# Optimization experiments

Measured on AMD Instinct MI355X. Metric: run time of the kernel, lower is better.

## Reference

```python
import jax, jax.numpy as jnp
import numpy as np

C = 256
HEADS = 8
HD = C // HEADS
SCALE = HD ** -0.5


def conv1x1(x, W, b):
    # x: [B,C_in,H,W], W: [C_out,C_in], b: [C_out]
    return jnp.einsum('oc,bchw->bohw', W, x) + b[None, :, None, None]


def setup_inputs() -> dict:
    key = jax.random.key(0)
    ks = jax.random.split(key, 12)
    B, H, Wd = 2, 48, 48
    s = C ** -0.5
    return {
        'x': jax.random.normal(ks[0], (B, C, H, Wd), jnp.float32),
        'uncertainty': jax.random.uniform(ks[1], (B, 1, H, Wd), jnp.float32),
        'Wq': jax.random.normal(ks[2], (C, C), jnp.float32) * s,
        'bq': jnp.zeros((C,), jnp.float32),
        'Wk': jax.random.normal(ks[3], (C, C), jnp.float32) * s,
        'bk': jnp.zeros((C,), jnp.float32),
        'Wv': jax.random.normal(ks[4], (C, C), jnp.float32) * s,
        'bv': jnp.zeros((C,), jnp.float32),
        'Wg': jax.random.normal(ks[5], (C, 1), jnp.float32),
        'bg': jnp.zeros((C,), jnp.float32),
        'Wo': jax.random.normal(ks[6], (C, C), jnp.float32) * s,
        'bo': jnp.zeros((C,), jnp.float32),
    }


def reference(x, uncertainty, Wq, bq, Wk, bk, Wv, bv, Wg, bg, Wo, bo):
    B, _, H, Wd = x.shape
    N = H * Wd
    # uncertainty gate (1x1 conv from 1 channel to C channels)
    uw = conv1x1(uncertainty, Wg, bg)            # [B,C,H,W]
    gated_x = x * (1.0 - uw)
    q = conv1x1(gated_x, Wq, bq).reshape(B, HEADS, HD, N)
    k = conv1x1(gated_x, Wk, bk).reshape(B, HEADS, HD, N)
    v = conv1x1(x, Wv, bv).reshape(B, HEADS, HD, N)
    # scores: [B,h,N,N] (query tokens n, key tokens m)
    scores = jnp.einsum('bhdn,bhdm->bhnm', q, k) * SCALE
    u_flat = uncertainty.reshape(B, 1, 1, N)      # mask over key axis
    scores = scores * (1.0 - u_flat)
    attn = jax.nn.softmax(scores, axis=-1)
    out = jnp.einsum('bhnm,bhdm->bhdn', attn, v)  # [B,h,hd,N]
    out = out.reshape(B, C, H, Wd)
    out = conv1x1(out, Wo, bo)
    return out + x
```

## Files before the change

### kernel.cpp

```cpp
#include <hip/hip_runtime.h>
#include <hip/hip_bf16.h>

typedef float f32x4 __attribute__((ext_vector_type(4)));
typedef __bf16 bf16x8 __attribute__((ext_vector_type(8)));
typedef __bf16 bf16x4 __attribute__((ext_vector_type(4)));
typedef short s16x4 __attribute__((ext_vector_type(4)));

constexpr int C = 256;
constexpr int N = 2304;
constexpr int T = 2 * N;

#if __has_builtin(__builtin_amdgcn_exp2f)
#define EXP2F(x) __builtin_amdgcn_exp2f(x)
#else
#define EXP2F(x) exp2f(x)
#endif

__device__ __forceinline__ bf16x8 load_bf8(const __bf16* p) {
    return *reinterpret_cast<const bf16x8*>(p);
}

__device__ __forceinline__ f32x4 mfma32(bf16x8 a, bf16x8 b, f32x4 c) {
    return __builtin_amdgcn_mfma_f32_16x16x32_bf16(a, b, c, 0, 0, 0);
}

#if __has_builtin(__builtin_amdgcn_mfma_f32_16x16x16bf16_1k)
__device__ __forceinline__ f32x4 mfma16(bf16x4 a, bf16x4 b, f32x4 c) {
    return __builtin_amdgcn_mfma_f32_16x16x16bf16_1k(
        __builtin_bit_cast(s16x4, a), __builtin_bit_cast(s16x4, b), c, 0, 0, 0);
}
#else
__device__ __forceinline__ f32x4 mfma16(bf16x4 a, bf16x4 b, f32x4 c) {
    f32x4 d;
    asm volatile("v_mfma_f32_16x16x16_bf16 %0, %1, %2, %3"
                 : "=v"(d) : "v"(a), "v"(b), "v"(c));
    return d;
}
#endif

__device__ __forceinline__ void gload_lds16(const __bf16* g, __bf16* l) {
    __builtin_amdgcn_global_load_lds(
        (const __attribute__((address_space(1))) void*)g,
        (__attribute__((address_space(3))) void*)l, 16, 0, 0);
}

#define VMCNT4() asm volatile("s_waitcnt vmcnt(4)" ::: "memory")
#define VMCNT0() asm volatile("s_waitcnt vmcnt(0)" ::: "memory")
#define LGKM0()  asm volatile("s_waitcnt lgkmcnt(0)" ::: "memory")

__global__ void wconv_kernel(const float* __restrict__ Wq, const float* __restrict__ Wk,
                             const float* __restrict__ Wv, const float* __restrict__ Wo,
                             __bf16* __restrict__ Wb) {
    const float* srcs[4] = {Wq, Wk, Wv, Wo};
    int m = blockIdx.x >> 6;
    int idx = (blockIdx.x & 63) * 256 + threadIdx.x;
    float4 v = reinterpret_cast<const float4*>(srcs[m])[idx];
    bf16x4 o = { (__bf16)v.x, (__bf16)v.y, (__bf16)v.z, (__bf16)v.w };
    reinterpret_cast<bf16x4*>(Wb + m * 65536)[idx] = o;
}

__global__ void prep_kernel(const float* __restrict__ x, const float* __restrict__ u,
                            const float* __restrict__ Wg, const float* __restrict__ bg,
                            __bf16* __restrict__ xT, __bf16* __restrict__ gxT) {
    __shared__ float tile[64][65];
    int b = blockIdx.z, c0 = blockIdx.y * 64, n0 = blockIdx.x * 64;
    int t = threadIdx.x;
    const float* xp = x + (b * C + c0) * N + n0;
    #pragma unroll
    for (int r = 0; r < 16; ++r) {
        int cl = r * 4 + (t >> 6);
        int nl = t & 63;
        tile[cl][nl] = xp[cl * N + nl];
    }
    __syncthreads();
    int cq = (t & 15) * 4;
    #pragma unroll
    for (int it = 0; it < 4; ++it) {
        int nl = it * 16 + (t >> 4);
        float uv = u[b * N + n0 + nl];
        bf16x4 xo, go;
        #pragma unroll
        for (int j = 0; j < 4; ++j) {
            int c = c0 + cq + j;
            float xv = tile[cq + j][nl];
            float gate = 1.0f - (Wg[c] * uv + bg[c]);
            xo[j] = (__bf16)xv;
            go[j] = (__bf16)(xv * gate);
        }
        int tok = b * N + n0 + nl;
        *reinterpret_cast<bf16x4*>(xT + (long)tok * C + c0 + cq) = xo;
        *reinterpret_cast<bf16x4*>(gxT + (long)tok * C + c0 + cq) = go;
    }
}

__global__ __launch_bounds__(256) void qkv_kernel(const __bf16* __restrict__ Wb,
    const __bf16* __restrict__ xT, const __bf16* __restrict__ gxT,
    const float* __restrict__ bq, const float* __restrict__ bk, const float* __restrict__ bv,
    const float* __restrict__ u,
    __bf16* __restrict__ Q, __bf16* __restrict__ K, __bf16* __restrict__ V) {
    int proj = blockIdx.z;
    int o0 = blockIdx.y * 64;
    int t0 = blockIdx.x * 32;
    int wave = threadIdx.x >> 6, lane = threadIdx.x & 63;
    int g = lane >> 4, r = lane & 15;
    int ow = o0 + wave * 16;
    const __bf16* W = Wb + proj * 65536;
    const __bf16* inp = (proj == 2) ? xT : gxT;
    f32x4 acc[2] = {};
    for (int k = 0; k < 8; ++k) {
        bf16x8 a = load_bf8(W + (ow + r) * C + k * 32 + g * 8);
        #pragma unroll
        for (int tb = 0; tb < 2; ++tb) {
            bf16x8 bfr = load_bf8(inp + (long)(t0 + tb * 16 + r) * C + k * 32 + g * 8);
            acc[tb] = mfma32(a, bfr, acc[tb]);
        }
    }
    const float* bias = (proj == 0) ? bq : (proj == 1) ? bk : bv;
    float bvw[4];
    #pragma unroll
    for (int i = 0; i < 4; ++i) bvw[i] = bias[ow + g * 4 + i];
    int h = ow >> 5, d0 = (ow & 31) + g * 4;
    const float SC = 0.17677669529663687f * 1.4426950408889634f;
    #pragma unroll
    for (int tb = 0; tb < 2; ++tb) {
        int t = t0 + tb * 16 + r;
        int b = t / N, n = t % N;
        if (proj == 2) {
            #pragma unroll
            for (int i = 0; i < 4; ++i)
                V[((long)(b * 8 + h) * 32 + d0 + i) * N + n] = (__bf16)(acc[tb][i] + bvw[i]);
        } else {
            bf16x4 outv;
            if (proj == 1) {
                float scale = SC * (1.0f - u[t]);
                #pragma unroll
                for (int i = 0; i < 4; ++i) outv[i] = (__bf16)((acc[tb][i] + bvw[i]) * scale);
            } else {
                #pragma unroll
                for (int i = 0; i < 4; ++i) outv[i] = (__bf16)(acc[tb][i] + bvw[i]);
            }
            __bf16* dst = (proj == 0) ? Q : K;
            *reinterpret_cast<bf16x4*>(dst + ((long)(b * 8 + h) * N + n) * 32 + d0) = outv;
        }
    }
}

__global__ __launch_bounds__(128) void attn_kernel(const __bf16* __restrict__ Q,
    const __bf16* __restrict__ K, const __bf16* __restrict__ V,
    __bf16* __restrict__ aoT) {
    __shared__ __bf16 sK[3][2048];
    __shared__ __bf16 sV[3][2048];
    int id = blockIdx.x;
    int xcd = id & 7, j = id >> 3;
    int bh = xcd + 8 * (j / 72);
    int qblk = j % 72;
    int tid = threadIdx.x;
    int wave = tid >> 6, lane = tid & 63;
    int g = lane >> 4, r = lane & 15;
    int q0w = qblk * 32 + wave * 16;
    const __bf16* Qg = Q + (long)bh * N * 32;
    const __bf16* Kg = K + (long)bh * N * 32;
    const __bf16* Vg = V + (long)bh * 32 * N;
    bf16x8 qf = load_bf8(Qg + (q0w + r) * 32 + g * 8);
    long ka = (long)tid * 8;
    int rrA = tid >> 3;
    int clA = (tid & 7) ^ ((tid >> 4) & 7);
    long va = (long)rrA * N + clA * 8;
    int so = wave * 512;
    auto STAGE = [&](long m0, __bf16* kd, __bf16* vd) {
        gload_lds16(Kg + m0 * 32 + ka,          kd + so);
        gload_lds16(Kg + m0 * 32 + 1024 + ka,   kd + 1024 + so);
        gload_lds16(Vg + va + m0,               vd + so);
        gload_lds16(Vg + va + 16 * N + m0,      vd + 1024 + so);
    };
    __bf16 *kA = &sK[0][0], *kB = &sK[1][0], *kC = &sK[2][0];
    __bf16 *vA = &sV[0][0], *vB = &sV[1][0], *vC = &sV[2][0];
    bf16x4 onesv;
    #pragma unroll
    for (int i = 0; i < 4; ++i) onesv[i] = (__bf16)1.0f;
    f32x4 oa0 = {}, oa1 = {}, oal = {};
    STAGE(0, kA, vA);
    STAGE(64, kB, vB);
    int k2r = (r >> 1) & 7;
    for (int t = 0; t < 36; ++t) {
        LGKM0();
        if (t < 34) { VMCNT4(); } else { VMCNT0(); }
        __builtin_amdgcn_s_barrier();
        if (t < 34) STAGE((long)(t + 2) * 64, kC, vC);
        bf16x8 kc0 = load_bf8(kA + (0 * 16 + r) * 32 + g * 8);
        bf16x8 kc1 = load_bf8(kA + (1 * 16 + r) * 32 + g * 8);
        bf16x8 kc2 = load_bf8(kA + (2 * 16 + r) * 32 + g * 8);
        bf16x8 kc3 = load_bf8(kA + (3 * 16 + r) * 32 + g * 8);
        bf16x4 vf[4][2];
        #pragma unroll
        for (int tt = 0; tt < 4; ++tt) {
            int pg = (((tt * 2 + (g >> 1)) ^ k2r) << 1) | (g & 1);
            #pragma unroll
            for (int dt = 0; dt < 2; ++dt)
                vf[tt][dt] = *reinterpret_cast<const bf16x4*>(
                    vA + (dt * 16 + r) * 64 + pg * 4);
        }
        f32x4 z = {};
        __builtin_amdgcn_s_setprio(1);
        f32x4 s0 = mfma32(kc0, qf, z);
        f32x4 s1 = mfma32(kc1, qf, z);
        f32x4 s2 = mfma32(kc2, qf, z);
        f32x4 s3 = mfma32(kc3, qf, z);
        __builtin_amdgcn_s_setprio(0);
        bf16x4 pa0, pa1, pa2, pa3;
        #pragma unroll
        for (int i = 0; i < 4; ++i) pa0[i] = (__bf16)EXP2F(s0[i]);
        #pragma unroll
        for (int i = 0; i < 4; ++i) pa1[i] = (__bf16)EXP2F(s1[i]);
        #pragma unroll
        for (int i = 0; i < 4; ++i) pa2[i] = (__bf16)EXP2F(s2[i]);
        #pragma unroll
        for (int i = 0; i < 4; ++i) pa3[i] = (__bf16)EXP2F(s3[i]);
        __builtin_amdgcn_s_setprio(1);
        oa0 = mfma16(vf[0][0], pa0, oa0);
        oa1 = mfma16(vf[0][1], pa0, oa1);
        oal = mfma16(onesv,    pa0, oal);
        oa0 = mfma16(vf[1][0], pa1, oa0);
        oa1 = mfma16(vf[1][1], pa1, oa1);
        oal = mfma16(onesv,    pa1, oal);
        oa0 = mfma16(vf[2][0], pa2, oa0);
        oa1 = mfma16(vf[2][1], pa2, oa1);
        oal = mfma16(onesv,    pa2, oal);
        oa0 = mfma16(vf[3][0], pa3, oa0);
        oa1 = mfma16(vf[3][1], pa3, oa1);
        oal = mfma16(onesv,    pa3, oal);
        __builtin_amdgcn_s_setprio(0);
        __bf16* tk = kA; kA = kB; kB = kC; kC = tk;
        __bf16* tv = vA; vA = vB; vB = vC; vC = tv;
    }
    float inv = 1.0f / oal[0];
    int b = bh >> 3, h = bh & 7;
    long tok = (long)b * N + q0w + r;
    bf16x4 ov0, ov1;
    #pragma unroll
    for (int i = 0; i < 4; ++i) ov0[i] = (__bf16)(oa0[i] * inv);
    #pragma unroll
    for (int i = 0; i < 4; ++i) ov1[i] = (__bf16)(oa1[i] * inv);
    *reinterpret_cast<bf16x4*>(aoT + tok * C + h * 32 + g * 4) = ov0;
    *reinterpret_cast<bf16x4*>(aoT + tok * C + h * 32 + 16 + g * 4) = ov1;
}

__global__ __launch_bounds__(256) void outp_kernel(const __bf16* __restrict__ Wb,
    const __bf16* __restrict__ aoT, const float* __restrict__ bo,
    const float* __restrict__ x, float* __restrict__ out) {
    int o0 = blockIdx.y * 64;
    int t0 = blockIdx.x * 32;
    int wave = threadIdx.x >> 6, lane = threadIdx.x & 63;
    int g = lane >> 4, r = lane & 15;
    int ow = o0 + wave * 16;
    const __bf16* W = Wb + 3 * 65536;
    f32x4 acc[2] = {};
    for (int k = 0; k < 8; ++k) {
        bf16x8 a = load_bf8(W + (ow + r) * C + k * 32 + g * 8);
        #pragma unroll
        for (int tb = 0; tb < 2; ++tb) {
            bf16x8 bfr = load_bf8(aoT + (long)(t0 + tb * 16 + r) * C + k * 32 + g * 8);
            acc[tb] = mfma32(a, bfr, acc[tb]);
        }
    }
    float bvw[4];
    #pragma unroll
    for (int i = 0; i < 4; ++i) bvw[i] = bo[ow + g * 4 + i];
    #pragma unroll
    for (int tb = 0; tb < 2; ++tb) {
        int t = t0 + tb * 16 + r;
        int b = t / N, n = t % N;
        #pragma unroll
        for (int i = 0; i < 4; ++i) {
            long idx = ((long)b * C + ow + g * 4 + i) * N + n;
            out[idx] = acc[tb][i] + bvw[i] + x[idx];
        }
    }
}

extern "C" void kernel_launch(void* const* d_in, const int* in_sizes, int n_in,
                              void* d_out, int out_size, void* d_ws, size_t ws_size,
                              hipStream_t stream) {
    const float* x  = (const float*)d_in[0];
    const float* u  = (const float*)d_in[1];
    const float* Wq = (const float*)d_in[2];
    const float* bq = (const float*)d_in[3];
    const float* Wk = (const float*)d_in[4];
    const float* bk = (const float*)d_in[5];
    const float* Wv = (const float*)d_in[6];
    const float* bv = (const float*)d_in[7];
    const float* Wg = (const float*)d_in[8];
    const float* bg = (const float*)d_in[9];
    const float* Wo = (const float*)d_in[10];
    const float* bo = (const float*)d_in[11];
    float* out = (float*)d_out;

    char* ws = (char*)d_ws;
    size_t off = 0;
    auto alloc = [&](size_t bytes) {
        char* p = ws + off;
        off += (bytes + 255) & ~(size_t)255;
        return p;
    };
    __bf16* Wb  = (__bf16*)alloc((size_t)4 * 65536 * 2);
    __bf16* xT  = (__bf16*)alloc((size_t)T * C * 2);
    __bf16* gxT = (__bf16*)alloc((size_t)T * C * 2);
    __bf16* Qb  = (__bf16*)alloc((size_t)16 * N * 32 * 2);
    __bf16* Kb  = (__bf16*)alloc((size_t)16 * N * 32 * 2);
    __bf16* Vb  = (__bf16*)alloc((size_t)16 * N * 32 * 2);
    __bf16* aoT = (__bf16*)alloc((size_t)T * C * 2);

    wconv_kernel<<<256, 256, 0, stream>>>(Wq, Wk, Wv, Wo, Wb);
    prep_kernel<<<dim3(36, 4, 2), 256, 0, stream>>>(x, u, Wg, bg, xT, gxT);
    qkv_kernel<<<dim3(144, 4, 3), 256, 0, stream>>>(Wb, xT, gxT, bq, bk, bv, u, Qb, Kb, Vb);
    attn_kernel<<<1152, 128, 0, stream>>>(Qb, Kb, Vb, aoT);
    outp_kernel<<<dim3(144, 4), 256, 0, stream>>>(Wb, aoT, bo, x, out);
}
```

Measured before the change: 78.97 us.

## Split attention key range across wave pairs and shrink prep/outp tiles

The attention kernel now runs 256 threads per block. Two wave pairs each process half of the key sequence with their own double-buffered LDS stages, and their partial outputs and row sums are combined through LDS at the end. This gives each block more parallelism and shortens the serial loop, at the cost of an extra reduction, a full vmcnt(0) wait each iteration instead of a three-stage pipeline, and larger LDS use. The prep and output projection kernels are also retiled to smaller per-block work so more blocks launch.

```diff
diff --git a/kernel.cpp b/kernel.cpp
--- a/kernel.cpp
+++ b/kernel.cpp
@@ -44,7 +44,6 @@
         (__attribute__((address_space(3))) void*)l, 16, 0, 0);
 }
 
-#define VMCNT4() asm volatile("s_waitcnt vmcnt(4)" ::: "memory")
 #define VMCNT0() asm volatile("s_waitcnt vmcnt(0)" ::: "memory")
 #define LGKM0()  asm volatile("s_waitcnt lgkmcnt(0)" ::: "memory")
 
@@ -62,21 +61,21 @@
 __global__ void prep_kernel(const float* __restrict__ x, const float* __restrict__ u,
                             const float* __restrict__ Wg, const float* __restrict__ bg,
                             __bf16* __restrict__ xT, __bf16* __restrict__ gxT) {
-    __shared__ float tile[64][65];
-    int b = blockIdx.z, c0 = blockIdx.y * 64, n0 = blockIdx.x * 64;
+    __shared__ float tile[32][65];
+    int b = blockIdx.z, c0 = blockIdx.y * 32, n0 = blockIdx.x * 64;
     int t = threadIdx.x;
     const float* xp = x + (b * C + c0) * N + n0;
     #pragma unroll
-    for (int r = 0; r < 16; ++r) {
+    for (int r = 0; r < 8; ++r) {
         int cl = r * 4 + (t >> 6);
         int nl = t & 63;
         tile[cl][nl] = xp[cl * N + nl];
     }
     __syncthreads();
-    int cq = (t & 15) * 4;
-    #pragma unroll
-    for (int it = 0; it < 4; ++it) {
-        int nl = it * 16 + (t >> 4);
+    int cq = (t & 7) * 4;
+    #pragma unroll
+    for (int it = 0; it < 2; ++it) {
+        int nl = it * 32 + (t >> 3);
         float uv = u[b * N + n0 + nl];
         bf16x4 xo, go;
         #pragma unroll
@@ -145,52 +144,57 @@
     }
 }
 
-__global__ __launch_bounds__(128) void attn_kernel(const __bf16* __restrict__ Q,
+__global__ __launch_bounds__(256) void attn_kernel(const __bf16* __restrict__ Q,
     const __bf16* __restrict__ K, const __bf16* __restrict__ V,
     __bf16* __restrict__ aoT) {
-    __shared__ __bf16 sK[3][2048];
-    __shared__ __bf16 sV[3][2048];
+    __shared__ __bf16 sK[2][2][2048];
+    __shared__ __bf16 sV[2][2][2048];
     int id = blockIdx.x;
     int xcd = id & 7, j = id >> 3;
     int bh = xcd + 8 * (j / 72);
     int qblk = j % 72;
     int tid = threadIdx.x;
     int wave = tid >> 6, lane = tid & 63;
+    int wp = wave & 1, pair = wave >> 1;
     int g = lane >> 4, r = lane & 15;
-    int q0w = qblk * 32 + wave * 16;
+    int q0 = qblk * 32;
     const __bf16* Qg = Q + (long)bh * N * 32;
-    const __bf16* Kg = K + (long)bh * N * 32;
-    const __bf16* Vg = V + (long)bh * 32 * N;
-    bf16x8 qf = load_bf8(Qg + (q0w + r) * 32 + g * 8);
-    long ka = (long)tid * 8;
-    int rrA = tid >> 3;
-    int clA = (tid & 7) ^ ((tid >> 4) & 7);
-    long va = (long)rrA * N + clA * 8;
-    int so = wave * 512;
+    const __bf16* Kg = K + (long)bh * N * 32 + (long)pair * 1152 * 32;
+    const __bf16* Vg = V + (long)bh * 32 * N + pair * 1152;
+    bf16x8 qf = load_bf8(Qg + (q0 + wp * 16 + r) * 32 + g * 8);
+    long ksrc = (long)(wp * 64 + lane) * 8;
+    int rr1 = wp * 8 + (lane >> 3);
+    long vsrc0 = (long)rr1 * N + ((lane & 7) ^ ((rr1 >> 1) & 7)) * 8;
+    int rr2 = 16 + rr1;
+    long vsrc1 = (long)rr2 * N + ((lane & 7) ^ ((rr2 >> 1) & 7)) * 8;
+    __bf16* kb0 = &sK[pair][0][0];
+    __bf16* kb1 = &sK[pair][1][0];
+    __bf16* vb0 = &sV[pair][0][0];
+    __bf16* vb1 = &sV[pair][1][0];
     auto STAGE = [&](long m0, __bf16* kd, __bf16* vd) {
-        gload_lds16(Kg + m0 * 32 + ka,          kd + so);
-        gload_lds16(Kg + m0 * 32 + 1024 + ka,   kd + 1024 + so);
-        gload_lds16(Vg + va + m0,               vd + so);
-        gload_lds16(Vg + va + 16 * N + m0,      vd + 1024 + so);
+        gload_lds16(Kg + m0 * 32 + ksrc,        kd + wp * 512);
+        gload_lds16(Kg + m0 * 32 + 1024 + ksrc, kd + 1024 + wp * 512);
+        gload_lds16(Vg + vsrc0 + m0,            vd + wp * 512);
+        gload_lds16(Vg + vsrc1 + m0,            vd + 1024 + wp * 512);
     };
-    __bf16 *kA = &sK[0][0], *kB = &sK[1][0], *kC = &sK[2][0];
-    __bf16 *vA = &sV[0][0], *vB = &sV[1][0], *vC = &sV[2][0];
     bf16x4 onesv;
     #pragma unroll
     for (int i = 0; i < 4; ++i) onesv[i] = (__bf16)1.0f;
     f32x4 oa0 = {}, oa1 = {}, oal = {};
-    STAGE(0, kA, vA);
-    STAGE(64, kB, vB);
     int k2r = (r >> 1) & 7;
-    for (int t = 0; t < 36; ++t) {
+    STAGE(0, kb0, vb0);
+    for (int t = 0; t < 18; ++t) {
         LGKM0();
-        if (t < 34) { VMCNT4(); } else { VMCNT0(); }
+        VMCNT0();
         __builtin_amdgcn_s_barrier();
-        if (t < 34) STAGE((long)(t + 2) * 64, kC, vC);
-        bf16x8 kc0 = load_bf8(kA + (0 * 16 + r) * 32 + g * 8);
-        bf16x8 kc1 = load_bf8(kA + (1 * 16 + r) * 32 + g * 8);
-        bf16x8 kc2 = load_bf8(kA + (2 * 16 + r) * 32 + g * 8);
-        bf16x8 kc3 = load_bf8(kA + (3 * 16 + r) * 32 + g * 8);
+        const __bf16* kb = (t & 1) ? kb1 : kb0;
+        const __bf16* vb = (t & 1) ? vb1 : vb0;
+        if (t < 17)
+            STAGE((long)(t + 1) * 64, (t & 1) ? kb0 : kb1, (t & 1) ? vb0 : vb1);
+        bf16x8 kc0 = load_bf8(kb + (0 * 16 + r) * 32 + g * 8);
+        bf16x8 kc1 = load_bf8(kb + (1 * 16 + r) * 32 + g * 8);
+        bf16x8 kc2 = load_bf8(kb + (2 * 16 + r) * 32 + g * 8);
+        bf16x8 kc3 = load_bf8(kb + (3 * 16 + r) * 32 + g * 8);
         bf16x4 vf[4][2];
         #pragma unroll
         for (int tt = 0; tt < 4; ++tt) {
@@ -198,7 +202,7 @@
             #pragma unroll
             for (int dt = 0; dt < 2; ++dt)
                 vf[tt][dt] = *reinterpret_cast<const bf16x4*>(
-                    vA + (dt * 16 + r) * 64 + pg * 4);
+                    vb + (dt * 16 + r) * 64 + pg * 4);
         }
         f32x4 z = {};
         __builtin_amdgcn_s_setprio(1);
@@ -230,51 +234,60 @@
         oa1 = mfma16(vf[3][1], pa3, oa1);
         oal = mfma16(onesv,    pa3, oal);
         __builtin_amdgcn_s_setprio(0);
-        __bf16* tk = kA; kA = kB; kB = kC; kC = tk;
-        __bf16* tv = vA; vA = vB; vB = vC; vC = tv;
-    }
-    float inv = 1.0f / oal[0];
-    int b = bh >> 3, h = bh & 7;
-    long tok = (long)b * N + q0w + r;
-    bf16x4 ov0, ov1;
-    #pragma unroll
-    for (int i = 0; i < 4; ++i) ov0[i] = (__bf16)(oa0[i] * inv);
-    #pragma unroll
-    for (int i = 0; i < 4; ++i) ov1[i] = (__bf16)(oa1[i] * inv);
-    *reinterpret_cast<bf16x4*>(aoT + tok * C + h * 32 + g * 4) = ov0;
-    *reinterpret_cast<bf16x4*>(aoT + tok * C + h * 32 + 16 + g * 4) = ov1;
+    }
+    __builtin_amdgcn_s_barrier();
+    float* F = reinterpret_cast<float*>(&sK[0][0][0]);
+    *reinterpret_cast<f32x4*>(F + wave * 512 + r * 32 + g * 4) = oa0;
+    *reinterpret_cast<f32x4*>(F + wave * 512 + r * 32 + 16 + g * 4) = oa1;
+    if (g == 0) F[2048 + wave * 16 + r] = oal[0];
+    __builtin_amdgcn_s_barrier();
+    if (tid < 128) {
+        int q = tid >> 2;
+        int wpq = q >> 4, qq = q & 15;
+        int d8 = (tid & 3) * 8;
+        int base0 = wpq * 512 + qq * 32 + d8;
+        int base1 = (wpq + 2) * 512 + qq * 32 + d8;
+        f32x4 a0 = *reinterpret_cast<f32x4*>(F + base0) +
+                   *reinterpret_cast<f32x4*>(F + base1);
+        f32x4 a1 = *reinterpret_cast<f32x4*>(F + base0 + 4) +
+                   *reinterpret_cast<f32x4*>(F + base1 + 4);
+        float l = F[2048 + wpq * 16 + qq] + F[2048 + (wpq + 2) * 16 + qq];
+        float inv = 1.0f / l;
+        bf16x8 ov;
+        #pragma unroll
+        for (int i = 0; i < 4; ++i) {
+            ov[i] = (__bf16)(a0[i] * inv);
+            ov[4 + i] = (__bf16)(a1[i] * inv);
+        }
+        int b = bh >> 3, h = bh & 7;
+        *reinterpret_cast<bf16x8*>(aoT + (long)(b * N + q0 + q) * C + h * 32 + d8) = ov;
+    }
 }
 
 __global__ __launch_bounds__(256) void outp_kernel(const __bf16* __restrict__ Wb,
     const __bf16* __restrict__ aoT, const float* __restrict__ bo,
     const float* __restrict__ x, float* __restrict__ out) {
     int o0 = blockIdx.y * 64;
-    int t0 = blockIdx.x * 32;
+    int t0 = blockIdx.x * 16;
     int wave = threadIdx.x >> 6, lane = threadIdx.x & 63;
     int g = lane >> 4, r = lane & 15;
     int ow = o0 + wave * 16;
     const __bf16* W = Wb + 3 * 65536;
-    f32x4 acc[2] = {};
+    f32x4 acc = {};
     for (int k = 0; k < 8; ++k) {
         bf16x8 a = load_bf8(W + (ow + r) * C + k * 32 + g * 8);
-        #pragma unroll
-        for (int tb = 0; tb < 2; ++tb) {
-            bf16x8 bfr = load_bf8(aoT + (long)(t0 + tb * 16 + r) * C + k * 32 + g * 8);
-            acc[tb] = mfma32(a, bfr, acc[tb]);
-        }
+        bf16x8 bfr = load_bf8(aoT + (long)(t0 + r) * C + k * 32 + g * 8);
+        acc = mfma32(a, bfr, acc);
     }
     float bvw[4];
     #pragma unroll
     for (int i = 0; i < 4; ++i) bvw[i] = bo[ow + g * 4 + i];
-    #pragma unroll
-    for (int tb = 0; tb < 2; ++tb) {
-        int t = t0 + tb * 16 + r;
-        int b = t / N, n = t % N;
-        #pragma unroll
-        for (int i = 0; i < 4; ++i) {
-            long idx = ((long)b * C + ow + g * 4 + i) * N + n;
-            out[idx] = acc[tb][i] + bvw[i] + x[idx];
-        }
+    int t = t0 + r;
+    int b = t / N, n = t % N;
+    #pragma unroll
+    for (int i = 0; i < 4; ++i) {
+        long idx = ((long)b * C + ow + g * 4 + i) * N + n;
+        out[idx] = acc[i] + bvw[i] + x[idx];
     }
 }
 
@@ -311,8 +324,8 @@
     __bf16* aoT = (__bf16*)alloc((size_t)T * C * 2);
 
     wconv_kernel<<<256, 256, 0, stream>>>(Wq, Wk, Wv, Wo, Wb);
-    prep_kernel<<<dim3(36, 4, 2), 256, 0, stream>>>(x, u, Wg, bg, xT, gxT);
+    prep_kernel<<<dim3(36, 8, 2), 256, 0, stream>>>(x, u, Wg, bg, xT, gxT);
     qkv_kernel<<<dim3(144, 4, 3), 256, 0, stream>>>(Wb, xT, gxT, bq, bk, bv, u, Qb, Kb, Vb);
-    attn_kernel<<<1152, 128, 0, stream>>>(Qb, Kb, Vb, aoT);
-    outp_kernel<<<dim3(144, 4), 256, 0, stream>>>(Wb, aoT, bo, x, out);
-}
+    attn_kernel<<<1152, 256, 0, stream>>>(Qb, Kb, Vb, aoT);
+    outp_kernel<<<dim3(288, 4), 256, 0, stream>>>(Wb, aoT, bo, x, out);
+}
```

Result: no change. 78.76 us (-0.3%).
